# Kernel optimization log

Hardware: AMD Instinct MI355X
Metric: run time of the kernel (lower is better)

The kernel has to match this reference:

```python
import jax, jax.numpy as jnp
import numpy as np

CUTOFF = 5.0
LOG2 = 0.6931471805599453

def ssp(x):
    # ShiftedSoftplus: softplus(x) - log(2)
    return jax.nn.softplus(x) - LOG2

def setup_inputs() -> dict:
    key = jax.random.key(0)
    ks = jax.random.split(key, 10)
    B, P, A, G, F, E = 2, 4096, 96, 1, 32, 20
    return {
        "scalar": jax.random.normal(ks[0], (B, A, G, F), jnp.float32),
        "scalar_reciever": jax.random.normal(ks[1], (B, P, G, F), jnp.float32),
        "expansion": jax.random.uniform(ks[2], (B, P, A, E), jnp.float32),
        "mask": jax.random.uniform(ks[3], (B, P, A, G), jnp.float32),
        "edge_distance": jax.random.uniform(ks[4], (B, P, A, 1), jnp.float32) * CUTOFF,
        "W1e": jax.random.normal(ks[5], (E, F), jnp.float32) * 0.1,
        "b1e": jnp.zeros((F,), jnp.float32),
        "W2e": jax.random.normal(ks[6], (F, F), jnp.float32) * 0.1,
        "b2e": jnp.zeros((F,), jnp.float32),
        "W1n": jax.random.normal(ks[7], (2 * F, F), jnp.float32) * 0.1,
        "b1n": jnp.zeros((F,), jnp.float32),
        "W2n": jax.random.normal(ks[8], (F, F), jnp.float32) * 0.1,
        "b2n": jnp.zeros((F,), jnp.float32),
    }

def reference(scalar, scalar_reciever, expansion, mask, edge_distance,
              W1e, b1e, W2e, b2e, W1n, b1n, W2n, b2n):
    F = scalar.shape[-1]
    # edge gate: 2-layer MLP on expansion, times soft cutoff  -> [B,P,A,F]
    gates = ssp(expansion @ W1e + b1e) @ W2e + b2e
    gates = gates * (1.0 - jax.nn.sigmoid(5.0 * (edge_distance - (CUTOFF - 1.5))))
    # pairwise node MLP: split first linear into source/target halves instead of
    # materializing the [B,P,A,G,2F] repeat+concat tensor (same math).
    Ws, Wt = W1n[:F], W1n[F:]
    src = jnp.einsum('bagf,fh->bagh', scalar, Ws)            # [B,A,G,H]
    tgt = jnp.einsum('bpgf,fh->bpgh', scalar_reciever, Wt)   # [B,P,G,H]
    h = src[:, None, :, :, :] + tgt[:, :, None, :, :] + b1n  # [B,P,A,G,H]
    nodes = ssp(h) @ W2n + b2n                               # [B,P,A,G,F]
    result = mask[..., None] * (gates[..., None, :] * nodes)
    return jnp.sum(result, axis=-3)                          # sum over atoms A -> [B,P,G,F]

if __name__ == "__main__":
    out = reference(**setup_inputs())
    print(out.shape)
```

## Files before the change

kernel.cpp:

```cpp
#include <hip/hip_runtime.h>

#define NB   2
#define NP   4096
#define NA   96
#define NF   32
#define NE   20
#define NBP  (NB*NP)

typedef __attribute__((ext_vector_type(8)))  short bf16x8;
typedef __attribute__((ext_vector_type(16))) float f32x16;

union Frag { bf16x8 v; int i[4]; };

__device__ __forceinline__ unsigned short f2bf(float x) {
  union { float f; unsigned u; } c; c.f = x;
  unsigned r = c.u + 0x7fffu + ((c.u >> 16) & 1u);
  return (unsigned short)(r >> 16);
}
__device__ __forceinline__ int pk2(float lo, float hi) {
  return (int)((unsigned)f2bf(lo) | ((unsigned)f2bf(hi) << 16));
}
__device__ __forceinline__ float ssp_f(float x) {
  float e = __expf(-fabsf(x));
  return fmaxf(x, 0.0f) + __logf(1.0f + e) - 0.69314718056f;
}
__device__ __forceinline__ f32x16 mfma32(const Frag a, const Frag b, f32x16 c) {
  return __builtin_amdgcn_mfma_f32_32x32x16_bf16(a.v, b.v, c, 0, 0, 0);
}
__device__ __forceinline__ f32x16 ld_bias16(const float* base ) {
  const float4* p = reinterpret_cast<const float4*>(base);
  float4 q0 = p[0], q1 = p[2], q2 = p[4], q3 = p[6];
  f32x16 c;
  c[0]=q0.x;  c[1]=q0.y;  c[2]=q0.z;  c[3]=q0.w;
  c[4]=q1.x;  c[5]=q1.y;  c[6]=q1.z;  c[7]=q1.w;
  c[8]=q2.x;  c[9]=q2.y;  c[10]=q2.z; c[11]=q2.w;
  c[12]=q3.x; c[13]=q3.y; c[14]=q3.z; c[15]=q3.w;
  return c;
}

__global__ __launch_bounds__(256)
void prep_kernel(const float* __restrict__ scalar,
                 const float* __restrict__ sr,
                 const float* __restrict__ W1n,
                 const float* __restrict__ b1n,
                 float* __restrict__ tgt_out,
                 float* __restrict__ src_ws)
{
  int i = blockIdx.x * 256 + threadIdx.x;
  int f = i & 31;
  int row = i >> 5;
  if (row < NBP) {
    const float* x = sr + row * NF;
    float a = 0.0f;
#pragma unroll
    for (int k = 0; k < NF; ++k) a = fmaf(x[k], W1n[(NF + k) * NF + f], a);
    tgt_out[i] = a;
  } else {
    int ba = row - NBP;
    const float* x = scalar + ba * NF;
    float a = b1n[f];
#pragma unroll
    for (int k = 0; k < NF; ++k) a = fmaf(x[k], W1n[k * NF + f], a);
    src_ws[ba * NF + f] = a;
  }
}

__global__ __launch_bounds__(64, 3)
void fused_main(const float* __restrict__ expansion,
                const float* __restrict__ mask,
                const float* __restrict__ edge_dist,
                const float* __restrict__ W1e,
                const float* __restrict__ b1e,
                const float* __restrict__ W2e,
                const float* __restrict__ b2e,
                const float* __restrict__ W2n,
                const float* __restrict__ b2n,
                const float* __restrict__ src_ws,
                float* out)
{
  const int lane = threadIdx.x;
  const int col  = lane & 31;
  const int hw   = lane >> 5;

  __shared__ __align__(16) float smb[128];
  if (lane < 32) {
    smb[lane]      = b1e[lane];
    smb[32 + lane] = b2e[lane];
    smb[64 + lane] = b2n[lane];
  }
  __syncthreads();

  Frag a1s0, a1s1, a2s0, a2s1, a3s0, a3s1;
#pragma unroll
  for (int r = 0; r < 4; ++r) {
    const int k0 = 8 * hw + 2 * r;
    const int k1 = 16 + k0;
    a1s0.i[r] = pk2(W1e[k0 * NF + col], W1e[(k0 + 1) * NF + col]);
    {
      int klo = (k1     < NE) ? k1     : (NE - 1);
      int khi = (k1 + 1 < NE) ? k1 + 1 : (NE - 1);
      float lo = W1e[klo * NF + col];
      float hi = W1e[khi * NF + col];
      lo = (k1     < NE) ? lo : 0.0f;
      hi = (k1 + 1 < NE) ? hi : 0.0f;
      a1s1.i[r] = pk2(lo, hi);
    }
    a2s0.i[r] = pk2(W2e[k0 * NF + col], W2e[(k0 + 1) * NF + col]);
    a2s1.i[r] = pk2(W2e[k1 * NF + col], W2e[(k1 + 1) * NF + col]);
    a3s0.i[r] = pk2(W2n[k0 * NF + col], W2n[(k0 + 1) * NF + col]);
    a3s1.i[r] = pk2(W2n[k1 * NF + col], W2n[(k1 + 1) * NF + col]);
  }

  const float* biasA = smb      + 4 * hw;
  const float* biasB = smb + 32 + 4 * hw;
  const float* biasC = smb + 64 + 4 * hw;

#pragma unroll 1
  for (int pi = 0; pi < 2; ++pi) {
    const int bp = blockIdx.x * 2 + pi;
    const int b  = bp >> 12;

    const float* tg = out + bp * NF;
    float4 t0 = *reinterpret_cast<const float4*>(tg + 8 * hw);
    float4 t1 = *reinterpret_cast<const float4*>(tg + 8 * hw + 4);
    float4 t2 = *reinterpret_cast<const float4*>(tg + 16 + 8 * hw);
    float4 t3 = *reinterpret_cast<const float4*>(tg + 16 + 8 * hw + 4);

    const float* expb  = expansion + (size_t)bp * (NA * NE);
    const float* maskb = mask      + bp * NA;
    const float* distb = edge_dist + bp * NA;
    const float* srcb  = src_ws    + b * (NA * NF);

    f32x16 acc;
#pragma unroll
    for (int r = 0; r < 16; ++r) acc[r] = 0.0f;

#pragma unroll 1
    for (int t = 0; t < 3; ++t) {
      const int a = t * 32 + col;

      const float* ea = expb + a * NE;
      float4 e0 = *reinterpret_cast<const float4*>(ea + 8 * hw);
      float4 e1 = *reinterpret_cast<const float4*>(ea + 8 * hw + 4);
      float4 e2 = *reinterpret_cast<const float4*>(ea + 16);
      Frag b1f0, b1f1;
      b1f0.i[0] = pk2(e0.x, e0.y);
      b1f0.i[1] = pk2(e0.z, e0.w);
      b1f0.i[2] = pk2(e1.x, e1.y);
      b1f0.i[3] = pk2(e1.z, e1.w);
      b1f1.i[0] = hw ? 0 : pk2(e2.x, e2.y);
      b1f1.i[1] = hw ? 0 : pk2(e2.z, e2.w);
      b1f1.i[2] = 0;
      b1f1.i[3] = 0;

      f32x16 d1 = ld_bias16(biasA);
      d1 = mfma32(a1s0, b1f0, d1);
      d1 = mfma32(a1s1, b1f1, d1);
#pragma unroll
      for (int r = 0; r < 16; ++r) d1[r] = ssp_f(d1[r]);

      int u0 = pk2(d1[0],  d1[1]);
      int u1 = pk2(d1[2],  d1[3]);
      int u2 = pk2(d1[4],  d1[5]);
      int u3 = pk2(d1[6],  d1[7]);
      int u4 = pk2(d1[8],  d1[9]);
      int u5 = pk2(d1[10], d1[11]);
      int u6 = pk2(d1[12], d1[13]);
      int u7 = pk2(d1[14], d1[15]);
      asm("v_permlane32_swap_b32 %0, %1" : "+v"(u0), "+v"(u2));
      asm("v_permlane32_swap_b32 %0, %1" : "+v"(u1), "+v"(u3));
      asm("v_permlane32_swap_b32 %0, %1" : "+v"(u4), "+v"(u6));
      asm("v_permlane32_swap_b32 %0, %1" : "+v"(u5), "+v"(u7));
      Frag b2f0, b2f1;
      b2f0.i[0] = u0; b2f0.i[1] = u1; b2f0.i[2] = u2; b2f0.i[3] = u3;
      b2f1.i[0] = u4; b2f1.i[1] = u5; b2f1.i[2] = u6; b2f1.i[3] = u7;

      f32x16 d2 = ld_bias16(biasB);
      d2 = mfma32(a2s0, b2f0, d2);
      d2 = mfma32(a2s1, b2f1, d2);

      const float mk = maskb[a];
      const float dd = distb[a];
      const float em = mk / (1.0f + __expf(5.0f * (dd - 3.5f)));

      const float* sa = srcb + a * NF;
      float4 s0 = *reinterpret_cast<const float4*>(sa + 8 * hw);
      float4 s1 = *reinterpret_cast<const float4*>(sa + 8 * hw + 4);
      float4 s2 = *reinterpret_cast<const float4*>(sa + 16 + 8 * hw);
      float4 s3 = *reinterpret_cast<const float4*>(sa + 16 + 8 * hw + 4);
      Frag b3f0, b3f1;
      b3f0.i[0] = pk2(ssp_f(s0.x + t0.x), ssp_f(s0.y + t0.y));
      b3f0.i[1] = pk2(ssp_f(s0.z + t0.z), ssp_f(s0.w + t0.w));
      b3f0.i[2] = pk2(ssp_f(s1.x + t1.x), ssp_f(s1.y + t1.y));
      b3f0.i[3] = pk2(ssp_f(s1.z + t1.z), ssp_f(s1.w + t1.w));
      b3f1.i[0] = pk2(ssp_f(s2.x + t2.x), ssp_f(s2.y + t2.y));
      b3f1.i[1] = pk2(ssp_f(s2.z + t2.z), ssp_f(s2.w + t2.w));
      b3f1.i[2] = pk2(ssp_f(s3.x + t3.x), ssp_f(s3.y + t3.y));
      b3f1.i[3] = pk2(ssp_f(s3.z + t3.z), ssp_f(s3.w + t3.w));

      f32x16 d3 = ld_bias16(biasC);
      d3 = mfma32(a3s0, b3f0, d3);
      d3 = mfma32(a3s1, b3f1, d3);

#pragma unroll
      for (int r = 0; r < 16; ++r) acc[r] = fmaf(em * d2[r], d3[r], acc[r]);
    }

#pragma unroll
    for (int m = 1; m <= 16; m <<= 1) {
#pragma unroll
      for (int r = 0; r < 16; ++r) acc[r] += __shfl_xor(acc[r], m, 64);
    }

    __syncthreads();
    if (col == 0) {
#pragma unroll
      for (int r = 0; r < 16; ++r)
        smb[96 + ((r & 3) + 8 * (r >> 2) + 4 * hw)] = acc[r];
    }
    __syncthreads();
    if (lane < 32) out[bp * NF + lane] = smb[96 + lane];
  }
}

extern "C" void kernel_launch(void* const* d_in, const int* in_sizes, int n_in,
                              void* d_out, int out_size, void* d_ws, size_t ws_size,
                              hipStream_t stream) {
  const float* scalar    = (const float*)d_in[0];
  const float* sreciever = (const float*)d_in[1];
  const float* expansion = (const float*)d_in[2];
  const float* maskp     = (const float*)d_in[3];
  const float* edist     = (const float*)d_in[4];
  const float* W1e       = (const float*)d_in[5];
  const float* b1e       = (const float*)d_in[6];
  const float* W2e       = (const float*)d_in[7];
  const float* b2e       = (const float*)d_in[8];
  const float* W1n       = (const float*)d_in[9];
  const float* b1n       = (const float*)d_in[10];
  const float* W2n       = (const float*)d_in[11];
  const float* b2n       = (const float*)d_in[12];
  float* out    = (float*)d_out;
  float* src_ws = (float*)d_ws;

  prep_kernel<<<1048, 256, 0, stream>>>(scalar, sreciever, W1n, b1n, out, src_ws);
  fused_main<<<NBP / 2, 64, 0, stream>>>(expansion, maskp, edist,
                                         W1e, b1e, W2e, b2e, W2n, b2n,
                                         src_ws, out);
}
```

Baseline: 155.9 us.

## Fuse target projection into main kernel, use 4-wave blocks and hardware bf16 pack

```diff
diff --git a/kernel.cpp b/kernel.cpp
--- a/kernel.cpp
+++ b/kernel.cpp
@@ -12,22 +12,19 @@
 
 union Frag { bf16x8 v; int i[4]; };
 
-__device__ __forceinline__ unsigned short f2bf(float x) {
-  union { float f; unsigned u; } c; c.f = x;
-  unsigned r = c.u + 0x7fffu + ((c.u >> 16) & 1u);
-  return (unsigned short)(r >> 16);
-}
-__device__ __forceinline__ int pk2(float lo, float hi) {
-  return (int)((unsigned)f2bf(lo) | ((unsigned)f2bf(hi) << 16));
+__device__ __forceinline__ int cvtpk(float lo, float hi) {
+  int r;
+  asm("v_cvt_pk_bf16_f32 %0, %1, %2" : "=v"(r) : "v"(lo), "v"(hi));
+  return r;
 }
 __device__ __forceinline__ float ssp_f(float x) {
-  float e = __expf(-fabsf(x));
-  return fmaxf(x, 0.0f) + __logf(1.0f + e) - 0.69314718056f;
+  float t = __expf(-fabsf(x));
+  return fmaxf(x, 0.0f) + __logf(1.0f + t) - 0.69314718056f;
 }
 __device__ __forceinline__ f32x16 mfma32(const Frag a, const Frag b, f32x16 c) {
   return __builtin_amdgcn_mfma_f32_32x32x16_bf16(a.v, b.v, c, 0, 0, 0);
 }
-__device__ __forceinline__ f32x16 ld_bias16(const float* base ) {
+__device__ __forceinline__ f32x16 ld_bias16(const float* __restrict__ base ) {
   const float4* p = reinterpret_cast<const float4*>(base);
   float4 q0 = p[0], q1 = p[2], q2 = p[4], q3 = p[6];
   f32x16 c;
@@ -39,33 +36,22 @@
 }
 
 __global__ __launch_bounds__(256)
-void prep_kernel(const float* __restrict__ scalar,
-                 const float* __restrict__ sr,
-                 const float* __restrict__ W1n,
-                 const float* __restrict__ b1n,
-                 float* __restrict__ tgt_out,
-                 float* __restrict__ src_ws)
+void prep_src(const float* __restrict__ scalar,
+              const float* __restrict__ W1n,
+              const float* __restrict__ b1n,
+              float* __restrict__ src_ws)
 {
   int i = blockIdx.x * 256 + threadIdx.x;
-  int f = i & 31;
-  int row = i >> 5;
-  if (row < NBP) {
-    const float* x = sr + row * NF;
-    float a = 0.0f;
-#pragma unroll
-    for (int k = 0; k < NF; ++k) a = fmaf(x[k], W1n[(NF + k) * NF + f], a);
-    tgt_out[i] = a;
-  } else {
-    int ba = row - NBP;
-    const float* x = scalar + ba * NF;
-    float a = b1n[f];
-#pragma unroll
-    for (int k = 0; k < NF; ++k) a = fmaf(x[k], W1n[k * NF + f], a);
-    src_ws[ba * NF + f] = a;
-  }
-}
-
-__global__ __launch_bounds__(64, 3)
+  int f  = i & 31;
+  int ba = i >> 5;
+  const float* x = scalar + ba * NF;
+  float a = b1n[f];
+#pragma unroll
+  for (int k = 0; k < NF; ++k) a = fmaf(x[k], W1n[k * NF + f], a);
+  src_ws[i] = a;
+}
+
+__global__ __launch_bounds__(256, 3)
 void fused_main(const float* __restrict__ expansion,
                 const float* __restrict__ mask,
                 const float* __restrict__ edge_dist,
@@ -75,56 +61,54 @@
                 const float* __restrict__ b2e,
                 const float* __restrict__ W2n,
                 const float* __restrict__ b2n,
+                const float* __restrict__ sr,
+                const float* __restrict__ W1n,
                 const float* __restrict__ src_ws,
-                float* out)
+                float* __restrict__ out)
 {
-  const int lane = threadIdx.x;
+  const int tid  = threadIdx.x;
+  const int wid  = tid >> 6;
+  const int lane = tid & 63;
   const int col  = lane & 31;
   const int hw   = lane >> 5;
-
-  __shared__ __align__(16) float smb[128];
-  if (lane < 32) {
-    smb[lane]      = b1e[lane];
-    smb[32 + lane] = b2e[lane];
-    smb[64 + lane] = b2n[lane];
-  }
-  __syncthreads();
 
   Frag a1s0, a1s1, a2s0, a2s1, a3s0, a3s1;
 #pragma unroll
   for (int r = 0; r < 4; ++r) {
     const int k0 = 8 * hw + 2 * r;
     const int k1 = 16 + k0;
-    a1s0.i[r] = pk2(W1e[k0 * NF + col], W1e[(k0 + 1) * NF + col]);
+    a1s0.i[r] = cvtpk(W1e[k0 * NF + col], W1e[(k0 + 1) * NF + col]);
     {
-      int klo = (k1     < NE) ? k1     : (NE - 1);
-      int khi = (k1 + 1 < NE) ? k1 + 1 : (NE - 1);
-      float lo = W1e[klo * NF + col];
-      float hi = W1e[khi * NF + col];
-      lo = (k1     < NE) ? lo : 0.0f;
-      hi = (k1 + 1 < NE) ? hi : 0.0f;
-      a1s1.i[r] = pk2(lo, hi);
-    }
-    a2s0.i[r] = pk2(W2e[k0 * NF + col], W2e[(k0 + 1) * NF + col]);
-    a2s1.i[r] = pk2(W2e[k1 * NF + col], W2e[(k1 + 1) * NF + col]);
-    a3s0.i[r] = pk2(W2n[k0 * NF + col], W2n[(k0 + 1) * NF + col]);
-    a3s1.i[r] = pk2(W2n[k1 * NF + col], W2n[(k1 + 1) * NF + col]);
+      float lo = (k1     < NE) ? W1e[k1 * NF + col]       : 0.0f;
+      float hi = (k1 + 1 < NE) ? W1e[(k1 + 1) * NF + col] : 0.0f;
+      a1s1.i[r] = cvtpk(lo, hi);
+    }
+    a2s0.i[r] = cvtpk(W2e[k0 * NF + col], W2e[(k0 + 1) * NF + col]);
+    a2s1.i[r] = cvtpk(W2e[k1 * NF + col], W2e[(k1 + 1) * NF + col]);
+    a3s0.i[r] = cvtpk(W2n[k0 * NF + col], W2n[(k0 + 1) * NF + col]);
+    a3s1.i[r] = cvtpk(W2n[k1 * NF + col], W2n[(k1 + 1) * NF + col]);
   }
 
-  const float* biasA = smb      + 4 * hw;
-  const float* biasB = smb + 32 + 4 * hw;
-  const float* biasC = smb + 64 + 4 * hw;
+  float wt[16];
+#pragma unroll
+  for (int i2 = 0; i2 < 16; ++i2) wt[i2] = W1n[(NF + 16 * hw + i2) * NF + col];
 
 #pragma unroll 1
   for (int pi = 0; pi < 2; ++pi) {
-    const int bp = blockIdx.x * 2 + pi;
+    const int bp = blockIdx.x * 8 + wid * 2 + pi;
     const int b  = bp >> 12;
 
-    const float* tg = out + bp * NF;
-    float4 t0 = *reinterpret_cast<const float4*>(tg + 8 * hw);
-    float4 t1 = *reinterpret_cast<const float4*>(tg + 8 * hw + 4);
-    float4 t2 = *reinterpret_cast<const float4*>(tg + 16 + 8 * hw);
-    float4 t3 = *reinterpret_cast<const float4*>(tg + 16 + 8 * hw + 4);
+    const float* srow = sr + bp * NF + 16 * hw;
+    float ts = 0.0f;
+#pragma unroll
+    for (int i2 = 0; i2 < 16; ++i2) ts = fmaf(srow[i2], wt[i2], ts);
+    ts += __shfl_xor(ts, 32, 64);
+    float tA[8], tB[8];
+#pragma unroll
+    for (int j = 0; j < 8; ++j) {
+      tA[j] = __shfl(ts,      8 * hw + j, 64);
+      tB[j] = __shfl(ts, 16 + 8 * hw + j, 64);
+    }
 
     const float* expb  = expansion + (size_t)bp * (NA * NE);
     const float* maskb = mask      + bp * NA;
@@ -144,29 +128,29 @@
       float4 e1 = *reinterpret_cast<const float4*>(ea + 8 * hw + 4);
       float4 e2 = *reinterpret_cast<const float4*>(ea + 16);
       Frag b1f0, b1f1;
-      b1f0.i[0] = pk2(e0.x, e0.y);
-      b1f0.i[1] = pk2(e0.z, e0.w);
-      b1f0.i[2] = pk2(e1.x, e1.y);
-      b1f0.i[3] = pk2(e1.z, e1.w);
-      b1f1.i[0] = hw ? 0 : pk2(e2.x, e2.y);
-      b1f1.i[1] = hw ? 0 : pk2(e2.z, e2.w);
+      b1f0.i[0] = cvtpk(e0.x, e0.y);
+      b1f0.i[1] = cvtpk(e0.z, e0.w);
+      b1f0.i[2] = cvtpk(e1.x, e1.y);
+      b1f0.i[3] = cvtpk(e1.z, e1.w);
+      b1f1.i[0] = hw ? 0 : cvtpk(e2.x, e2.y);
+      b1f1.i[1] = hw ? 0 : cvtpk(e2.z, e2.w);
       b1f1.i[2] = 0;
       b1f1.i[3] = 0;
 
-      f32x16 d1 = ld_bias16(biasA);
+      f32x16 d1 = ld_bias16(b1e + 4 * hw);
       d1 = mfma32(a1s0, b1f0, d1);
       d1 = mfma32(a1s1, b1f1, d1);
 #pragma unroll
       for (int r = 0; r < 16; ++r) d1[r] = ssp_f(d1[r]);
 
-      int u0 = pk2(d1[0],  d1[1]);
-      int u1 = pk2(d1[2],  d1[3]);
-      int u2 = pk2(d1[4],  d1[5]);
-      int u3 = pk2(d1[6],  d1[7]);
-      int u4 = pk2(d1[8],  d1[9]);
-      int u5 = pk2(d1[10], d1[11]);
-      int u6 = pk2(d1[12], d1[13]);
-      int u7 = pk2(d1[14], d1[15]);
+      int u0 = cvtpk(d1[0],  d1[1]);
+      int u1 = cvtpk(d1[2],  d1[3]);
+      int u2 = cvtpk(d1[4],  d1[5]);
+      int u3 = cvtpk(d1[6],  d1[7]);
+      int u4 = cvtpk(d1[8],  d1[9]);
+      int u5 = cvtpk(d1[10], d1[11]);
+      int u6 = cvtpk(d1[12], d1[13]);
+      int u7 = cvtpk(d1[14], d1[15]);
       asm("v_permlane32_swap_b32 %0, %1" : "+v"(u0), "+v"(u2));
       asm("v_permlane32_swap_b32 %0, %1" : "+v"(u1), "+v"(u3));
       asm("v_permlane32_swap_b32 %0, %1" : "+v"(u4), "+v"(u6));
@@ -175,13 +159,14 @@
       b2f0.i[0] = u0; b2f0.i[1] = u1; b2f0.i[2] = u2; b2f0.i[3] = u3;
       b2f1.i[0] = u4; b2f1.i[1] = u5; b2f1.i[2] = u6; b2f1.i[3] = u7;
 
-      f32x16 d2 = ld_bias16(biasB);
+      f32x16 d2 = ld_bias16(b2e + 4 * hw);
       d2 = mfma32(a2s0, b2f0, d2);
       d2 = mfma32(a2s1, b2f1, d2);
 
       const float mk = maskb[a];
       const float dd = distb[a];
-      const float em = mk / (1.0f + __expf(5.0f * (dd - 3.5f)));
+      const float z  = __expf(5.0f * (dd - 3.5f));
+      const float em = mk * __builtin_amdgcn_rcpf(1.0f + z);
 
       const float* sa = srcb + a * NF;
       float4 s0 = *reinterpret_cast<const float4*>(sa + 8 * hw);
@@ -189,16 +174,16 @@
       float4 s2 = *reinterpret_cast<const float4*>(sa + 16 + 8 * hw);
       float4 s3 = *reinterpret_cast<const float4*>(sa + 16 + 8 * hw + 4);
       Frag b3f0, b3f1;
-      b3f0.i[0] = pk2(ssp_f(s0.x + t0.x), ssp_f(s0.y + t0.y));
-      b3f0.i[1] = pk2(ssp_f(s0.z + t0.z), ssp_f(s0.w + t0.w));
-      b3f0.i[2] = pk2(ssp_f(s1.x + t1.x), ssp_f(s1.y + t1.y));
-      b3f0.i[3] = pk2(ssp_f(s1.z + t1.z), ssp_f(s1.w + t1.w));
-      b3f1.i[0] = pk2(ssp_f(s2.x + t2.x), ssp_f(s2.y + t2.y));
-      b3f1.i[1] = pk2(ssp_f(s2.z + t2.z), ssp_f(s2.w + t2.w));
-      b3f1.i[2] = pk2(ssp_f(s3.x + t3.x), ssp_f(s3.y + t3.y));
-      b3f1.i[3] = pk2(ssp_f(s3.z + t3.z), ssp_f(s3.w + t3.w));
-
-      f32x16 d3 = ld_bias16(biasC);
+      b3f0.i[0] = cvtpk(ssp_f(s0.x + tA[0]), ssp_f(s0.y + tA[1]));
+      b3f0.i[1] = cvtpk(ssp_f(s0.z + tA[2]), ssp_f(s0.w + tA[3]));
+      b3f0.i[2] = cvtpk(ssp_f(s1.x + tA[4]), ssp_f(s1.y + tA[5]));
+      b3f0.i[3] = cvtpk(ssp_f(s1.z + tA[6]), ssp_f(s1.w + tA[7]));
+      b3f1.i[0] = cvtpk(ssp_f(s2.x + tB[0]), ssp_f(s2.y + tB[1]));
+      b3f1.i[1] = cvtpk(ssp_f(s2.z + tB[2]), ssp_f(s2.w + tB[3]));
+      b3f1.i[2] = cvtpk(ssp_f(s3.x + tB[4]), ssp_f(s3.y + tB[5]));
+      b3f1.i[3] = cvtpk(ssp_f(s3.z + tB[6]), ssp_f(s3.w + tB[7]));
+
+      f32x16 d3 = ld_bias16(b2n + 4 * hw);
       d3 = mfma32(a3s0, b3f0, d3);
       d3 = mfma32(a3s1, b3f1, d3);
 
@@ -212,14 +197,16 @@
       for (int r = 0; r < 16; ++r) acc[r] += __shfl_xor(acc[r], m, 64);
     }
 
-    __syncthreads();
     if (col == 0) {
-#pragma unroll
-      for (int r = 0; r < 16; ++r)
-        smb[96 + ((r & 3) + 8 * (r >> 2) + 4 * hw)] = acc[r];
-    }
-    __syncthreads();
-    if (lane < 32) out[bp * NF + lane] = smb[96 + lane];
+      float4* o = reinterpret_cast<float4*>(out + bp * NF);
+#pragma unroll
+      for (int q = 0; q < 4; ++q) {
+        float4 v;
+        v.x = acc[4 * q];     v.y = acc[4 * q + 1];
+        v.z = acc[4 * q + 2]; v.w = acc[4 * q + 3];
+        o[2 * q + hw] = v;
+      }
+    }
   }
 }
 
@@ -242,8 +229,8 @@
   float* out    = (float*)d_out;
   float* src_ws = (float*)d_ws;
 
-  prep_kernel<<<1048, 256, 0, stream>>>(scalar, sreciever, W1n, b1n, out, src_ws);
-  fused_main<<<NBP / 2, 64, 0, stream>>>(expansion, maskp, edist,
-                                         W1e, b1e, W2e, b2e, W2n, b2n,
-                                         src_ws, out);
-}
+  prep_src<<<24, 256, 0, stream>>>(scalar, W1n, b1n, src_ws);
+  fused_main<<<NBP / 8, 256, 0, stream>>>(expansion, maskp, edist,
+                                          W1e, b1e, W2e, b2e, W2n, b2n,
+                                          sreciever, W1n, src_ws, out);
+}
```

After: 167.1 us. +7.2%, slower.
